# Optimization experiments

Hardware: AMD Instinct MI355X
Metric: run time of the kernel (lower is better)

## Reference

```python
import jax, jax.numpy as jnp
import numpy as np

# Keras Normalization adaption stats for n_neighbors=15 (2*15 = 30 channels)
NORM_MEAN = jnp.array([-3.7189561e-06, 0.000286194, 0.0020740835, 6.5275993, -0.0052857199,
                       10.554636, 0.057773598, 13.915789, 0.060970016, 16.840271,
                       0.0570364, 19.415283, 0.044104282, 21.721455, 0.11490919,
                       23.64683, 0.099816084, 25.365578, 0.01769533, 26.861437,
                       0.054662503, 28.197876, -0.0024771576, 29.295244, 0.039666731,
                       30.319246, 0.0088442909, 31.160933, -0.026727753, 31.874565], dtype=jnp.float32)
NORM_VAR = jnp.array([3.3091978e-06, 0.00016750646, 0.80988622, 85135.219, 1.5621265,
                      222580.2, 8.812871, 386912.78, 10.180468, 566622.44,
                      9.8600769, 753158.06, 7.8372045, 942701.62, 30.926426,
                      1117233.0, 25.045353, 1285543.9, 6.3646226, 1441639.1,
                      12.326629, 1588653.4, 6.9686499, 1714707.9, 10.755516,
                      1836677.8, 8.416419, 1940088.8, 10.344138, 2029969.6], dtype=jnp.float32)
BN_EPS = 1e-3  # keras BatchNormalization default epsilon


def _isc_dirac(x, bc_idx, bc_w, kernel, bias):
    """ConvDirac: barycentric gather-interpolate + rotated template correlation.
    x: (B,V,C); bc_idx/bc_w: (B,V,R,A,3); kernel: (R,A,T,C); bias: (T,)
    returns (B,V,O,T) with O = n_angular rotations (rotation_delta=1)."""
    contrib = jax.vmap(lambda s, i: s[i])(x, bc_idx)            # (B,V,R,A,3,C) gather within batch
    interp = jnp.einsum('bvrat,bvratc->bvrac', bc_w, contrib)    # barycentric interpolation
    n_ang = kernel.shape[1]
    rk = jnp.stack([jnp.roll(kernel, o, axis=1) for o in range(n_ang)])  # (O,R,A,T,C)
    return jax.nn.elu(jnp.einsum('oratc,bvrac->bvot', rk, interp) + bias)


def _amp(x):
    """AngularMaxPooling: pick rotation with maximal euclidean response. x: (B,V,O,T) -> (B,V,T)"""
    idx = jnp.argmax(jnp.linalg.norm(x, axis=-1), axis=-1)       # (B,V)
    return jnp.take_along_axis(x, idx[:, :, None, None], axis=2)[:, :, 0, :]


def _bn(x, gamma, beta):
    # inference-mode BatchNormalization with fresh moving stats (mean=0, var=1)
    return gamma * x * jax.lax.rsqrt(jnp.float32(1.0) + BN_EPS) + beta


def setup_inputs() -> dict:
    key = jax.random.key(0)
    B, V, R, A, K3, C_in = 4, 2048, 5, 8, 3, 30
    dims = [128, 128, 256]
    ks = jax.random.split(key, 16)
    # raw tangent-projection signal, drawn at the scale the adaption stats expect
    signal = NORM_MEAN + jax.random.normal(ks[0], (B, V, C_in), dtype=jnp.float32) * jnp.sqrt(NORM_VAR)
    bc_idx = jax.random.randint(ks[1], (B, V, R, A, K3), 0, V)
    bc_w = jax.random.uniform(ks[2], (B, V, R, A, K3), dtype=jnp.float32)
    bc_w = bc_w / bc_w.sum(axis=-1, keepdims=True)               # barycentric weights sum to 1

    def glorot(k, shape):
        fan = float(np.prod(shape[:-2]) * (shape[-1] + shape[-2])) if len(shape) == 4 else float(shape[0] + shape[1])
        return jax.random.normal(k, shape, dtype=jnp.float32) * jnp.sqrt(2.0 / fan)

    inp = {'signal': signal, 'bc_idx': bc_idx, 'bc_w': bc_w}
    c_prev = C_in
    for i, d in enumerate(dims):
        inp[f'k{i}'] = glorot(ks[3 + i], (R, A, d, c_prev))
        inp[f'b{i}'] = jnp.zeros((d,), jnp.float32)
        inp[f'g{i}'] = jnp.ones((d,), jnp.float32)
        inp[f'be{i}'] = jnp.zeros((d,), jnp.float32)
        c_prev = d
    inp['w1'] = glorot(ks[8], (256, 512)); inp['c1'] = jnp.zeros((512,), jnp.float32)
    inp['w2'] = glorot(ks[9], (512, 256)); inp['c2'] = jnp.zeros((256,), jnp.float32)
    inp['w3'] = glorot(ks[10], (256, 40)); inp['c3'] = jnp.zeros((40,), jnp.float32)
    return inp


def reference(signal, bc_idx, bc_w, k0, b0, g0, be0, k1, b1, g1, be1, k2, b2, g2, be2,
              w1, c1, w2, c2, w3, c3):
    x = (signal - NORM_MEAN) * jax.lax.rsqrt(NORM_VAR)           # input normalization
    for k, b, g, be in ((k0, b0, g0, be0), (k1, b1, g1, be1), (k2, b2, g2, be2)):
        x = _bn(_amp(_isc_dirac(x, bc_idx, bc_w, k, b)), g, be)  # dropout is identity in inference
    x = jnp.max(x, axis=1)                                       # GlobalMaxPool1D over vertices
    x = jax.nn.elu(x @ w1 + c1)
    x = jax.nn.elu(x @ w2 + c2)
    return x @ w3 + c3                                           # (B, 40) logits
```

## Files before the change

kernel.cpp:

```cpp
#include <hip/hip_runtime.h>
#include <hip/hip_bf16.h>
#include <math.h>

#define Bz 4
#define Vz 2048
#define RA 40

typedef short bf16x8 __attribute__((ext_vector_type(8)));
typedef float f32x4 __attribute__((ext_vector_type(4)));

__device__ __forceinline__ unsigned fasu(float f){ union{float f;unsigned u;}x;x.f=f;return x.u; }
__device__ __forceinline__ float usaf(unsigned u){ union{unsigned u;float f;}x;x.u=u;return x.f; }

__device__ __forceinline__ unsigned short f2bf(float f) {
    unsigned u = fasu(f);
    unsigned r = u + 0x7FFF + ((u >> 16) & 1);
    return (unsigned short)(r >> 16);
}
__device__ __forceinline__ float bf2f(unsigned short h) { return usaf(((unsigned)h) << 16); }

__constant__ float NORM_MEAN_C[30] = {
    -3.7189561e-06f, 0.000286194f, 0.0020740835f, 6.5275993f, -0.0052857199f,
    10.554636f, 0.057773598f, 13.915789f, 0.060970016f, 16.840271f,
    0.0570364f, 19.415283f, 0.044104282f, 21.721455f, 0.11490919f,
    23.64683f, 0.099816084f, 25.365578f, 0.01769533f, 26.861437f,
    0.054662503f, 28.197876f, -0.0024771576f, 29.295244f, 0.039666731f,
    30.319246f, 0.0088442909f, 31.160933f, -0.026727753f, 31.874565f};
__constant__ float NORM_VAR_C[30] = {
    3.3091978e-06f, 0.00016750646f, 0.80988622f, 85135.219f, 1.5621265f,
    222580.2f, 8.812871f, 386912.78f, 10.180468f, 566622.44f,
    9.8600769f, 753158.06f, 7.8372045f, 942701.62f, 30.926426f,
    1117233.0f, 25.045353f, 1285543.9f, 6.3646226f, 1441639.1f,
    12.326629f, 1588653.4f, 6.9686499f, 1714707.9f, 10.755516f,
    1836677.8f, 8.416419f, 1940088.8f, 10.344138f, 2029969.6f};

__device__ __forceinline__ float elu_f(float x) {
    return x > 0.f ? x : expm1f(x);
}

__device__ __forceinline__ unsigned encf(float f) {
    unsigned u = fasu(f);
    return (f < 0.f) ? ~u : (u | 0x80000000u);
}
__device__ __forceinline__ float decf(unsigned u) {
    return (u & 0x80000000u) ? usaf(u & 0x7FFFFFFFu) : usaf(~u);
}

template <int CROW, int T, int KB>
__device__ __forceinline__ void expand_body(int e, const float* __restrict__ kern,
                                            unsigned short* __restrict__ wt) {
    constexpr int CB = (CROW == 128) ? 4 : 1;
    int kb = e / (T * 32);
    int rem = e % (T * 32);
    int n = rem >> 5, kk = rem & 31;
    int par = kb & 1;
    int jp = (kb >> 1) & 3;
    int g = kb >> 3;
    int cblk = g % CB;
    int r = g / CB;
    int c = cblk * 32 + kk;
    float v = 0.f;
    if (c < CROW) {
        float k1 = kern[((size_t)((r * 8 + jp) * T + n)) * CROW + c];
        float k2 = kern[((size_t)((r * 8 + jp + 4) * T + n)) * CROW + c];
        v = 0.5f * (par == 0 ? (k1 + k2) : (k1 - k2));
    }
    unsigned short hi = f2bf(v);
    unsigned short lo = f2bf(v - bf2f(hi));
    size_t off = ((size_t)kb * 2) * T * 32 + (n >> 4) * 512 + (kk >> 3) * 128 + (n & 15) * 8 + (kk & 7);
    wt[off] = hi;
    wt[off + (size_t)T * 32] = lo;
}

__global__ void prep_k(const float* __restrict__ sig, float* __restrict__ x0,
                       const float* __restrict__ k0, unsigned short* __restrict__ wt0,
                       const float* __restrict__ k1, unsigned short* __restrict__ wt1,
                       const float* __restrict__ k2, unsigned short* __restrict__ wt2,
                       unsigned* __restrict__ gpool) {
    const int bid = blockIdx.x, tid = threadIdx.x;
    if (bid < 960) {
        int e = bid * 256 + tid;
        if (e < Bz * Vz * 30) {
            int c = e % 30;
            x0[e] = (sig[e] - NORM_MEAN_C[c]) * rsqrtf(NORM_VAR_C[c]);
        }
    } else if (bid < 1600) {
        int e = (bid - 960) * 256 + tid;
        if (e < 40 * 128 * 32) expand_body<30, 128, 40>(e, k0, wt0);
    } else if (bid < 4160) {
        int e = (bid - 1600) * 256 + tid;
        if (e < 160 * 128 * 32) expand_body<128, 128, 160>(e, k1, wt1);
    } else if (bid < 9280) {
        int e = (bid - 4160) * 256 + tid;
        if (e < 160 * 256 * 32) expand_body<128, 256, 160>(e, k2, wt2);
    } else {
        int e = (bid - 9280) * 256 + tid;
        if (e < Bz * 256) gpool[e] = 0u;
    }
}

template <int CROW, int T, int KB, int NW, bool FUSE, bool POOL>
__global__ __launch_bounds__(64 * NW) void conv_k(const float* __restrict__ x,
                                              const int* __restrict__ bc_idx,
                                              const float* __restrict__ bc_w,
                                              const unsigned short* __restrict__ wt,
                                              const float* __restrict__ bias,
                                              const float* __restrict__ g,
                                              const float* __restrict__ be,
                                              float* __restrict__ xout) {
    constexpr int CB = (CROW == 128) ? 4 : 1;
    constexpr int G = KB / 8;
    constexpr int CW = 2 * NW;
    constexpr int CPT = 32 / CW;
    __shared__ unsigned short Ih[2][4096], Il[2][4096];
    __shared__ float normp[64][NW];
    __shared__ int bo[8];
    __shared__ unsigned poolmax[64 * NW];
    const int tid = threadIdx.x;
    const int wid = tid >> 6, lane = tid & 63;
    const int fr = lane & 15, fq = lane >> 4;
    const int fr2 = fr >> 2, om_l = fr & 3;
    const int wn = wid * 64;
    const int m0 = blockIdx.y * 64;
    const int b = m0 >> 14;
    const float* xb_ = x + (size_t)b * Vz * CROW;
    const int* idxb = bc_idx + (size_t)b * Vz * RA * 3;
    const float* wb = bc_w + (size_t)b * Vz * RA * 3;

    const int cidx = tid % CW;
    const int jI = (tid / CW) & 3;
    const int vbI = tid / (CW * 4);
    const int vglob_b = ((m0 & 16383) >> 3) + vbI;
    const int wbase = vbI * 512 + ((cidx * CPT) >> 3) * 128 + ((cidx * CPT) & 7);
    const int nbase = wn >> 4;

    f32x4 acc[4][4] = {};

    auto store_split2 = [&](const float* vv, int buf, int sA, int sB, unsigned sgB) {
        unsigned hp[CPT / 2], lp[CPT / 2];
#pragma unroll
        for (int p2 = 0; p2 < CPT / 2; ++p2) {
            float v0 = vv[2 * p2], v1 = vv[2 * p2 + 1];
            unsigned u0 = fasu(v0), u1 = fasu(v1);
            unsigned h0 = u0 & 0xFFFF0000u, h1 = u1 & 0xFFFF0000u;
            float l0 = v0 - usaf(h0), l1 = v1 - usaf(h1);
            hp[p2] = (u0 >> 16) | h1;
            lp[p2] = (fasu(l0) >> 16) | (fasu(l1) & 0xFFFF0000u);
        }
        auto put = [&](int slot, unsigned sg) {
            const int sl = (slot & 8) | (((slot & 7) + 2 * (vbI & 3)) & 7);
            const int ad = wbase + sl * 8;
            if constexpr (CPT == 8) {
                *(uint4*)&Ih[buf][ad] = make_uint4(hp[0] ^ sg, hp[1] ^ sg, hp[2] ^ sg, hp[3] ^ sg);
                *(uint4*)&Il[buf][ad] = make_uint4(lp[0] ^ sg, lp[1] ^ sg, lp[2] ^ sg, lp[3] ^ sg);
            } else {
                *(uint2*)&Ih[buf][ad] = make_uint2(hp[0] ^ sg, hp[1] ^ sg);
                *(uint2*)&Il[buf][ad] = make_uint2(lp[0] ^ sg, lp[1] ^ sg);
            }
        };
        put(sA, 0u);
        put(sB, sgB);
    };

    int i_n0 = 0, i_n1 = 0, i_n2 = 0, i_n3 = 0, i_n4 = 0, i_n5 = 0;
    float w_n0 = 0.f, w_n1 = 0.f, w_n2 = 0.f, w_n3 = 0.f, w_n4 = 0.f, w_n5 = 0.f;
    {
        const int gi1 = (vglob_b * RA + jI) * 3;
        const int gi2 = gi1 + 12;
        int a0 = idxb[gi1], a1 = idxb[gi1 + 1], a2 = idxb[gi1 + 2];
        int a3 = idxb[gi2], a4 = idxb[gi2 + 1], a5 = idxb[gi2 + 2];
        float u0 = wb[gi1], u1 = wb[gi1 + 1], u2 = wb[gi1 + 2];
        float u3 = wb[gi2], u4 = wb[gi2 + 1], u5 = wb[gi2 + 2];
        float xj[CPT], xj4[CPT];
        const int cs0 = cidx * CPT;
        if (CROW == 128) {
            const float4* p0 = (const float4*)(xb_ + (size_t)a0 * CROW + cs0);
            const float4* p1 = (const float4*)(xb_ + (size_t)a1 * CROW + cs0);
            const float4* p2 = (const float4*)(xb_ + (size_t)a2 * CROW + cs0);
            const float4* p3 = (const float4*)(xb_ + (size_t)a3 * CROW + cs0);
            const float4* p4 = (const float4*)(xb_ + (size_t)a4 * CROW + cs0);
            const float4* p5 = (const float4*)(xb_ + (size_t)a5 * CROW + cs0);
#pragma unroll
            for (int qq = 0; qq < CPT / 4; ++qq) {
                float4 A = p0[qq], B = p1[qq], C = p2[qq];
                xj[qq * 4 + 0] = u0 * A.x + u1 * B.x + u2 * C.x;
                xj[qq * 4 + 1] = u0 * A.y + u1 * B.y + u2 * C.y;
                xj[qq * 4 + 2] = u0 * A.z + u1 * B.z + u2 * C.z;
                xj[qq * 4 + 3] = u0 * A.w + u1 * B.w + u2 * C.w;
                float4 D = p3[qq], E = p4[qq], F = p5[qq];
                xj4[qq * 4 + 0] = u3 * D.x + u4 * E.x + u5 * F.x;
                xj4[qq * 4 + 1] = u3 * D.y + u4 * E.y + u5 * F.y;
                xj4[qq * 4 + 2] = u3 * D.z + u4 * E.z + u5 * F.z;
                xj4[qq * 4 + 3] = u3 * D.w + u4 * E.w + u5 * F.w;
            }
        } else {
#pragma unroll
            for (int cc = 0; cc < CPT; ++cc) {
                int c = cs0 + cc;
                bool ok = (c < CROW);
                xj[cc] = ok ? (u0 * xb_[(size_t)a0 * CROW + c] + u1 * xb_[(size_t)a1 * CROW + c] + u2 * xb_[(size_t)a2 * CROW + c]) : 0.f;
                xj4[cc] = ok ? (u3 * xb_[(size_t)a3 * CROW + c] + u4 * xb_[(size_t)a4 * CROW + c] + u5 * xb_[(size_t)a5 * CROW + c]) : 0.f;
            }
        }
#pragma unroll
        for (int cc = 0; cc < CPT; ++cc) {
            float a_ = xj[cc], b_ = xj4[cc];
            xj[cc] = a_ + b_;
            xj4[cc] = a_ - b_;
        }
        store_split2(xj, 0, jI, jI + 4, 0u);
        store_split2(xj4, 0, 8 + jI, 12 + jI, 0x80008000u);
        if (G > 1) {
            const int rn = 1 / CB;
            const int gi1n = (vglob_b * RA + rn * 8 + jI) * 3;
            const int gi2n = gi1n + 12;
            i_n0 = idxb[gi1n]; i_n1 = idxb[gi1n + 1]; i_n2 = idxb[gi1n + 2];
            i_n3 = idxb[gi2n]; i_n4 = idxb[gi2n + 1]; i_n5 = idxb[gi2n + 2];
            w_n0 = wb[gi1n]; w_n1 = wb[gi1n + 1]; w_n2 = wb[gi1n + 2];
            w_n3 = wb[gi2n]; w_n4 = wb[gi2n + 1]; w_n5 = wb[gi2n + 2];
        }
    }
    __syncthreads();

    for (int gidx = 0; gidx < G; ++gidx) {
        const bool hn = (gidx + 1 < G);
        const int ni0 = i_n0, ni1 = i_n1, ni2 = i_n2, ni3 = i_n3, ni4 = i_n4, ni5 = i_n5;
        const float mw0 = w_n0, mw1 = w_n1, mw2 = w_n2, mw3 = w_n3, mw4 = w_n4, mw5 = w_n5;
        const int bgn = gidx + 1;
        const int cs_n = (bgn % CB) * 32 + cidx * CPT;
        const int ibuf = gidx & 1;
        float4 qa0[CPT / 4], qa1[CPT / 4], qa2[CPT / 4];
        float4 qb0[CPT / 4], qb1[CPT / 4], qb2[CPT / 4];
        float sg[6][CPT];
        float xj[CPT], xj4[CPT];
#pragma unroll
        for (int ap = 0; ap < 8; ++ap) {
            const int jp = ap >> 1, par = ap & 1;
            const int kb = gidx * 8 + ap;
            const unsigned short* bb = wt + ((size_t)kb * 2) * (T * 32) +
                                       (size_t)nbase * 512 + lane * 8;
            bf16x8 bh[4], bl[4];
#pragma unroll
            for (int nj = 0; nj < 4; ++nj) {
                bh[nj] = *(const bf16x8*)(bb + nj * 512);
                bl[nj] = *(const bf16x8*)(bb + (size_t)T * 32 + nj * 512);
            }
            const int sp = (jp + om_l + 2 * fr2) & 7;
            const int sl = par * 8 + sp;
            bf16x8 ah[2], al[2];
#pragma unroll
            for (int miq = 0; miq < 2; ++miq) {
                const int ad = (miq * 4 + fr2) * 512 + fq * 128 + sl * 8;
                ah[miq] = *(const bf16x8*)&Ih[ibuf][ad];
                al[miq] = *(const bf16x8*)&Il[ibuf][ad];
            }
            __builtin_amdgcn_s_setprio(1);
#pragma unroll
            for (int miq = 0; miq < 2; ++miq)
#pragma unroll
                for (int nj = 0; nj < 4; ++nj) {
                    const int mi = par * 2 + miq;
                    acc[mi][nj] = __builtin_amdgcn_mfma_f32_16x16x32_bf16(ah[miq], bh[nj], acc[mi][nj], 0, 0, 0);
                    acc[mi][nj] = __builtin_amdgcn_mfma_f32_16x16x32_bf16(ah[miq], bl[nj], acc[mi][nj], 0, 0, 0);
                    acc[mi][nj] = __builtin_amdgcn_mfma_f32_16x16x32_bf16(al[miq], bh[nj], acc[mi][nj], 0, 0, 0);
                }
            __builtin_amdgcn_s_setprio(0);
            if (hn) {
                if (ap == 0) {
                    if (CROW == 128) {
                        const float4* p0 = (const float4*)(xb_ + (size_t)ni0 * CROW + cs_n);
                        const float4* p1 = (const float4*)(xb_ + (size_t)ni1 * CROW + cs_n);
                        const float4* p2 = (const float4*)(xb_ + (size_t)ni2 * CROW + cs_n);
#pragma unroll
                        for (int qq = 0; qq < CPT / 4; ++qq) { qa0[qq] = p0[qq]; qa1[qq] = p1[qq]; qa2[qq] = p2[qq]; }
                    } else {
#pragma unroll
                        for (int cc = 0; cc < CPT; ++cc) {
                            int c = cs_n + cc;
                            bool ok = (c < CROW);
                            sg[0][cc] = ok ? xb_[(size_t)ni0 * CROW + c] : 0.f;
                            sg[1][cc] = ok ? xb_[(size_t)ni1 * CROW + c] : 0.f;
                            sg[2][cc] = ok ? xb_[(size_t)ni2 * CROW + c] : 0.f;
                        }
                    }
                } else if (ap == 1) {
                    if (CROW == 128) {
                        const float4* p3 = (const float4*)(xb_ + (size_t)ni3 * CROW + cs_n);
                        const float4* p4 = (const float4*)(xb_ + (size_t)ni4 * CROW + cs_n);
                        const float4* p5 = (const float4*)(xb_ + (size_t)ni5 * CROW + cs_n);
#pragma unroll
                        for (int qq = 0; qq < CPT / 4; ++qq) { qb0[qq] = p3[qq]; qb1[qq] = p4[qq]; qb2[qq] = p5[qq]; }
                    } else {
#pragma unroll
                        for (int cc = 0; cc < CPT; ++cc) {
                            int c = cs_n + cc;
                            bool ok = (c < CROW);
                            sg[3][cc] = ok ? xb_[(size_t)ni3 * CROW + c] : 0.f;
                            sg[4][cc] = ok ? xb_[(size_t)ni4 * CROW + c] : 0.f;
                            sg[5][cc] = ok ? xb_[(size_t)ni5 * CROW + c] : 0.f;
                        }
                    }
                } else if (ap == 2) {
                    if (gidx + 2 < G) {
                        const int rn = (gidx + 2) / CB;
                        const int gi1 = (vglob_b * RA + rn * 8 + jI) * 3;
                        const int gi2 = gi1 + 12;
                        i_n0 = idxb[gi1]; i_n1 = idxb[gi1 + 1]; i_n2 = idxb[gi1 + 2];
                        i_n3 = idxb[gi2]; i_n4 = idxb[gi2 + 1]; i_n5 = idxb[gi2 + 2];
                        w_n0 = wb[gi1]; w_n1 = wb[gi1 + 1]; w_n2 = wb[gi1 + 2];
                        w_n3 = wb[gi2]; w_n4 = wb[gi2 + 1]; w_n5 = wb[gi2 + 2];
                    }
                } else if (ap == 3) {
                    if (CROW == 128) {
#pragma unroll
                        for (int qq = 0; qq < CPT / 4; ++qq) {
                            float4 A = qa0[qq], B = qa1[qq], C = qa2[qq];
                            xj[qq * 4 + 0] = mw0 * A.x + mw1 * B.x + mw2 * C.x;
                            xj[qq * 4 + 1] = mw0 * A.y + mw1 * B.y + mw2 * C.y;
                            xj[qq * 4 + 2] = mw0 * A.z + mw1 * B.z + mw2 * C.z;
                            xj[qq * 4 + 3] = mw0 * A.w + mw1 * B.w + mw2 * C.w;
                        }
                    } else {
#pragma unroll
                        for (int cc = 0; cc < CPT; ++cc)
                            xj[cc] = mw0 * sg[0][cc] + mw1 * sg[1][cc] + mw2 * sg[2][cc];
                    }
                } else if (ap == 4) {
                    if (CROW == 128) {
#pragma unroll
                        for (int qq = 0; qq < CPT / 4; ++qq) {
                            float4 D = qb0[qq], E = qb1[qq], F = qb2[qq];
                            xj4[qq * 4 + 0] = mw3 * D.x + mw4 * E.x + mw5 * F.x;
                            xj4[qq * 4 + 1] = mw3 * D.y + mw4 * E.y + mw5 * F.y;
                            xj4[qq * 4 + 2] = mw3 * D.z + mw4 * E.z + mw5 * F.z;
                            xj4[qq * 4 + 3] = mw3 * D.w + mw4 * E.w + mw5 * F.w;
                        }
                    } else {
#pragma unroll
                        for (int cc = 0; cc < CPT; ++cc)
                            xj4[cc] = mw3 * sg[3][cc] + mw4 * sg[4][cc] + mw5 * sg[5][cc];
                    }
                } else if (ap == 5) {
#pragma unroll
                    for (int cc = 0; cc < CPT; ++cc) {
                        float a_ = xj[cc], b_ = xj4[cc];
                        xj[cc] = a_ + b_;
                        xj4[cc] = a_ - b_;
                    }
                } else if (ap == 6) {
                    store_split2(xj, ibuf ^ 1, jI, jI + 4, 0u);
                } else {
                    store_split2(xj4, ibuf ^ 1, 8 + jI, 12 + jI, 0x80008000u);
                }
            }
        }
        __syncthreads();
    }

    if (FUSE) {
        float ssP[2][4], ssM[2][4];
#pragma unroll
        for (int mg = 0; mg < 2; ++mg)
#pragma unroll
            for (int r = 0; r < 4; ++r) { ssP[mg][r] = 0.f; ssM[mg][r] = 0.f; }
#pragma unroll
        for (int mg = 0; mg < 2; ++mg)
#pragma unroll
            for (int nj = 0; nj < 4; ++nj)
#pragma unroll
                for (int r = 0; r < 4; ++r) {
                    const int t = wn + nj * 16 + fr;
                    float se = acc[mg][nj][r], so = acc[mg + 2][nj][r];
                    float vP = elu_f(se + so + bias[t]);
                    float vM = elu_f(se - so + bias[t]);
                    acc[mg][nj][r] = vP;
                    acc[mg + 2][nj][r] = vM;
                    ssP[mg][r] += vP * vP;
                    ssM[mg][r] += vM * vM;
                }
#pragma unroll
        for (int mg = 0; mg < 2; ++mg)
#pragma unroll
            for (int r = 0; r < 4; ++r) {
                float s1 = ssP[mg][r];
                s1 += __shfl_xor(s1, 1); s1 += __shfl_xor(s1, 2);
                s1 += __shfl_xor(s1, 4); s1 += __shfl_xor(s1, 8);
                float s2 = ssM[mg][r];
                s2 += __shfl_xor(s2, 1); s2 += __shfl_xor(s2, 2);
                s2 += __shfl_xor(s2, 4); s2 += __shfl_xor(s2, 8);
                if (fr == 0) {
                    normp[(mg * 4 + fq) * 8 + r][wid] = s1;
                    normp[(mg * 4 + fq) * 8 + r + 4][wid] = s2;
                }
            }
        __syncthreads();
        if (POOL) poolmax[tid] = 0u;
        if (tid < 8) {
            float best = -1.f; int bsel = 0;
#pragma unroll
            for (int oo = 0; oo < 8; ++oo) {
                float tot = 0.f;
#pragma unroll
                for (int wq = 0; wq < NW; ++wq) tot += normp[tid * 8 + oo][wq];
                if (tot > best) { best = tot; bsel = oo; }
            }
            bo[tid] = bsel;
        }
        __syncthreads();
        const float rsbn = rsqrtf(1.001f);
#pragma unroll
        for (int mg = 0; mg < 2; ++mg)
#pragma unroll
            for (int r = 0; r < 4; ++r) {
                const int vloc = mg * 4 + fq;
                const int bsel = bo[vloc];
                if (r == bsel) {
                    const int vg = (m0 >> 3) + vloc;
#pragma unroll
                    for (int nj = 0; nj < 4; ++nj) {
                        const int t = wn + nj * 16 + fr;
                        float f = acc[mg][nj][r] * g[t] * rsbn + be[t];
                        if (!POOL) xout[(size_t)vg * T + t] = f;
                        else atomicMax(&poolmax[t], encf(f));
                    }
                }
                if (r + 4 == bsel) {
                    const int vg = (m0 >> 3) + vloc;
#pragma unroll
                    for (int nj = 0; nj < 4; ++nj) {
                        const int t = wn + nj * 16 + fr;
                        float f = acc[mg + 2][nj][r] * g[t] * rsbn + be[t];
                        if (!POOL) xout[(size_t)vg * T + t] = f;
                        else atomicMax(&poolmax[t], encf(f));
                    }
                }
            }
        if (POOL) {
            __syncthreads();
            unsigned pv = poolmax[tid];
            if (pv) atomicMax((unsigned*)xout + (((size_t)b) << 8) + tid, pv);
        }
    }
}

__global__ __launch_bounds__(256) void head_k(const float* __restrict__ partial,
                                              const float* __restrict__ w1, const float* __restrict__ c1,
                                              const float* __restrict__ w2, const float* __restrict__ c2,
                                              const float* __restrict__ w3, const float* __restrict__ c3,
                                              float* __restrict__ outp) {
    __shared__ float p[256], h1s[512], h2s[256];
    const int b = blockIdx.x, tid = threadIdx.x;
    const unsigned* gp = (const unsigned*)partial;
    p[tid] = decf(gp[b * 256 + tid]);
    __syncthreads();
#pragma unroll
    for (int rep = 0; rep < 2; ++rep) {
        int n = rep * 256 + tid;
        float s = c1[n];
        for (int k = 0; k < 256; ++k) s += p[k] * w1[k * 512 + n];
        h1s[n] = elu_f(s);
    }
    __syncthreads();
    {
        float s = c2[tid];
        for (int k = 0; k < 512; ++k) s += h1s[k] * w2[k * 256 + tid];
        h2s[tid] = elu_f(s);
    }
    __syncthreads();
    if (tid < 40) {
        float s = c3[tid];
        for (int k = 0; k < 256; ++k) s += h2s[k] * w3[k * 40 + tid];
        outp[b * 40 + tid] = s;
    }
}

extern "C" void kernel_launch(void* const* d_in, const int* in_sizes, int n_in,
                              void* d_out, int out_size, void* d_ws, size_t ws_size,
                              hipStream_t stream) {
    const float* signal = (const float*)d_in[0];
    const int* bc_idx = (const int*)d_in[1];
    const float* bc_w = (const float*)d_in[2];
    const float* k0 = (const float*)d_in[3];
    const float* b0 = (const float*)d_in[4];
    const float* g0 = (const float*)d_in[5];
    const float* be0 = (const float*)d_in[6];
    const float* k1 = (const float*)d_in[7];
    const float* b1 = (const float*)d_in[8];
    const float* g1 = (const float*)d_in[9];
    const float* be1 = (const float*)d_in[10];
    const float* k2 = (const float*)d_in[11];
    const float* b2 = (const float*)d_in[12];
    const float* g2 = (const float*)d_in[13];
    const float* be2 = (const float*)d_in[14];
    const float* w1 = (const float*)d_in[15];
    const float* c1 = (const float*)d_in[16];
    const float* w2 = (const float*)d_in[17];
    const float* c2 = (const float*)d_in[18];
    const float* w3 = (const float*)d_in[19];
    const float* c3 = (const float*)d_in[20];
    float* outp = (float*)d_out;

    float* ws = (float*)d_ws;
    float* xa = ws;
    float* xb = xa + (size_t)8192 * 128;
    unsigned* gpool = (unsigned*)(xb + (size_t)8192 * 128);
    unsigned short* wt0 = (unsigned short*)(gpool + 4096);
    unsigned short* wt1 = wt0 + (size_t)40 * 2 * 128 * 32;
    unsigned short* wt2 = wt1 + (size_t)160 * 2 * 128 * 32;

    prep_k<<<9284, 256, 0, stream>>>(signal, xa, k0, wt0, k1, wt1, k2, wt2, gpool);

    conv_k<30, 128, 40, 2, true, false><<<dim3(1, 1024), 128, 0, stream>>>(
        xa, bc_idx, bc_w, wt0, b0, g0, be0, xb);

    conv_k<128, 128, 160, 2, true, false><<<dim3(1, 1024), 128, 0, stream>>>(
        xb, bc_idx, bc_w, wt1, b1, g1, be1, xa);

    conv_k<128, 256, 160, 4, true, true><<<dim3(1, 1024), 256, 0, stream>>>(
        xa, bc_idx, bc_w, wt2, b2, g2, be2, (float*)gpool);

    head_k<<<Bz, 256, 0, stream>>>((const float*)gpool, w1, c1, w2, c2, w3, c3, outp);
}
```

Before: 577.7 us.

## Process two M-tiles per block in layer-3 conv to reuse weight fragments

```diff
diff --git a/kernel.cpp b/kernel.cpp
--- a/kernel.cpp
+++ b/kernel.cpp
@@ -99,8 +99,8 @@
     }
 }
 
-template <int CROW, int T, int KB, int NW, bool FUSE, bool POOL>
-__global__ __launch_bounds__(64 * NW) void conv_k(const float* __restrict__ x,
+template <int CROW, int T, int KB, int NW, int MT, bool FUSE, bool POOL>
+__global__ __launch_bounds__(64 * NW, 2) void conv_k(const float* __restrict__ x,
                                               const int* __restrict__ bc_idx,
                                               const float* __restrict__ bc_w,
                                               const unsigned short* __restrict__ wt,
@@ -110,18 +110,18 @@
                                               float* __restrict__ xout) {
     constexpr int CB = (CROW == 128) ? 4 : 1;
     constexpr int G = KB / 8;
-    constexpr int CW = 2 * NW;
+    constexpr int CW = 2 * NW / MT;
     constexpr int CPT = 32 / CW;
-    __shared__ unsigned short Ih[2][4096], Il[2][4096];
-    __shared__ float normp[64][NW];
-    __shared__ int bo[8];
+    __shared__ unsigned short Ih[2][4096 * MT], Il[2][4096 * MT];
+    __shared__ float normp[64 * MT][NW];
+    __shared__ int bo[8 * MT];
     __shared__ unsigned poolmax[64 * NW];
     const int tid = threadIdx.x;
     const int wid = tid >> 6, lane = tid & 63;
     const int fr = lane & 15, fq = lane >> 4;
     const int fr2 = fr >> 2, om_l = fr & 3;
     const int wn = wid * 64;
-    const int m0 = blockIdx.y * 64;
+    const int m0 = blockIdx.y * (64 * MT);
     const int b = m0 >> 14;
     const float* xb_ = x + (size_t)b * Vz * CROW;
     const int* idxb = bc_idx + (size_t)b * Vz * RA * 3;
@@ -134,7 +134,7 @@
     const int wbase = vbI * 512 + ((cidx * CPT) >> 3) * 128 + ((cidx * CPT) & 7);
     const int nbase = wn >> 4;
 
-    f32x4 acc[4][4] = {};
+    f32x4 acc[MT][4][4] = {};
 
     auto store_split2 = [&](const float* vv, int buf, int sA, int sB, unsigned sgB) {
         unsigned hp[CPT / 2], lp[CPT / 2];
@@ -247,24 +247,27 @@
             }
             const int sp = (jp + om_l + 2 * fr2) & 7;
             const int sl = par * 8 + sp;
-            bf16x8 ah[2], al[2];
-#pragma unroll
-            for (int miq = 0; miq < 2; ++miq) {
-                const int ad = (miq * 4 + fr2) * 512 + fq * 128 + sl * 8;
-                ah[miq] = *(const bf16x8*)&Ih[ibuf][ad];
-                al[miq] = *(const bf16x8*)&Il[ibuf][ad];
-            }
-            __builtin_amdgcn_s_setprio(1);
-#pragma unroll
-            for (int miq = 0; miq < 2; ++miq)
-#pragma unroll
-                for (int nj = 0; nj < 4; ++nj) {
-                    const int mi = par * 2 + miq;
-                    acc[mi][nj] = __builtin_amdgcn_mfma_f32_16x16x32_bf16(ah[miq], bh[nj], acc[mi][nj], 0, 0, 0);
-                    acc[mi][nj] = __builtin_amdgcn_mfma_f32_16x16x32_bf16(ah[miq], bl[nj], acc[mi][nj], 0, 0, 0);
-                    acc[mi][nj] = __builtin_amdgcn_mfma_f32_16x16x32_bf16(al[miq], bh[nj], acc[mi][nj], 0, 0, 0);
+#pragma unroll
+            for (int mt = 0; mt < MT; ++mt) {
+                bf16x8 ah[2], al[2];
+#pragma unroll
+                for (int miq = 0; miq < 2; ++miq) {
+                    const int ad = mt * 4096 + (miq * 4 + fr2) * 512 + fq * 128 + sl * 8;
+                    ah[miq] = *(const bf16x8*)&Ih[ibuf][ad];
+                    al[miq] = *(const bf16x8*)&Il[ibuf][ad];
                 }
-            __builtin_amdgcn_s_setprio(0);
+                __builtin_amdgcn_s_setprio(1);
+#pragma unroll
+                for (int miq = 0; miq < 2; ++miq)
+#pragma unroll
+                    for (int nj = 0; nj < 4; ++nj) {
+                        const int mi = par * 2 + miq;
+                        acc[mt][mi][nj] = __builtin_amdgcn_mfma_f32_16x16x32_bf16(ah[miq], bh[nj], acc[mt][mi][nj], 0, 0, 0);
+                        acc[mt][mi][nj] = __builtin_amdgcn_mfma_f32_16x16x32_bf16(ah[miq], bl[nj], acc[mt][mi][nj], 0, 0, 0);
+                        acc[mt][mi][nj] = __builtin_amdgcn_mfma_f32_16x16x32_bf16(al[miq], bh[nj], acc[mt][mi][nj], 0, 0, 0);
+                    }
+                __builtin_amdgcn_s_setprio(0);
+            }
             if (hn) {
                 if (ap == 0) {
                     if (CROW == 128) {
@@ -358,44 +361,50 @@
     }
 
     if (FUSE) {
-        float ssP[2][4], ssM[2][4];
-#pragma unroll
-        for (int mg = 0; mg < 2; ++mg)
-#pragma unroll
-            for (int r = 0; r < 4; ++r) { ssP[mg][r] = 0.f; ssM[mg][r] = 0.f; }
-#pragma unroll
-        for (int mg = 0; mg < 2; ++mg)
-#pragma unroll
-            for (int nj = 0; nj < 4; ++nj)
+        float ssP[MT][2][4], ssM[MT][2][4];
+#pragma unroll
+        for (int mt = 0; mt < MT; ++mt)
+#pragma unroll
+            for (int mg = 0; mg < 2; ++mg)
+#pragma unroll
+                for (int r = 0; r < 4; ++r) { ssP[mt][mg][r] = 0.f; ssM[mt][mg][r] = 0.f; }
+#pragma unroll
+        for (int mt = 0; mt < MT; ++mt)
+#pragma unroll
+            for (int mg = 0; mg < 2; ++mg)
+#pragma unroll
+                for (int nj = 0; nj < 4; ++nj)
+#pragma unroll
+                    for (int r = 0; r < 4; ++r) {
+                        const int t = wn + nj * 16 + fr;
+                        float se = acc[mt][mg][nj][r], so = acc[mt][mg + 2][nj][r];
+                        float vP = elu_f(se + so + bias[t]);
+                        float vM = elu_f(se - so + bias[t]);
+                        acc[mt][mg][nj][r] = vP;
+                        acc[mt][mg + 2][nj][r] = vM;
+                        ssP[mt][mg][r] += vP * vP;
+                        ssM[mt][mg][r] += vM * vM;
+                    }
+#pragma unroll
+        for (int mt = 0; mt < MT; ++mt)
+#pragma unroll
+            for (int mg = 0; mg < 2; ++mg)
 #pragma unroll
                 for (int r = 0; r < 4; ++r) {
-                    const int t = wn + nj * 16 + fr;
-                    float se = acc[mg][nj][r], so = acc[mg + 2][nj][r];
-                    float vP = elu_f(se + so + bias[t]);
-                    float vM = elu_f(se - so + bias[t]);
-                    acc[mg][nj][r] = vP;
-                    acc[mg + 2][nj][r] = vM;
-                    ssP[mg][r] += vP * vP;
-                    ssM[mg][r] += vM * vM;
+                    float s1 = ssP[mt][mg][r];
+                    s1 += __shfl_xor(s1, 1); s1 += __shfl_xor(s1, 2);
+                    s1 += __shfl_xor(s1, 4); s1 += __shfl_xor(s1, 8);
+                    float s2 = ssM[mt][mg][r];
+                    s2 += __shfl_xor(s2, 1); s2 += __shfl_xor(s2, 2);
+                    s2 += __shfl_xor(s2, 4); s2 += __shfl_xor(s2, 8);
+                    if (fr == 0) {
+                        normp[(mt * 8 + mg * 4 + fq) * 8 + r][wid] = s1;
+                        normp[(mt * 8 + mg * 4 + fq) * 8 + r + 4][wid] = s2;
+                    }
                 }
-#pragma unroll
-        for (int mg = 0; mg < 2; ++mg)
-#pragma unroll
-            for (int r = 0; r < 4; ++r) {
-                float s1 = ssP[mg][r];
-                s1 += __shfl_xor(s1, 1); s1 += __shfl_xor(s1, 2);
-                s1 += __shfl_xor(s1, 4); s1 += __shfl_xor(s1, 8);
-                float s2 = ssM[mg][r];
-                s2 += __shfl_xor(s2, 1); s2 += __shfl_xor(s2, 2);
-                s2 += __shfl_xor(s2, 4); s2 += __shfl_xor(s2, 8);
-                if (fr == 0) {
-                    normp[(mg * 4 + fq) * 8 + r][wid] = s1;
-                    normp[(mg * 4 + fq) * 8 + r + 4][wid] = s2;
-                }
-            }
         __syncthreads();
         if (POOL) poolmax[tid] = 0u;
-        if (tid < 8) {
+        if (tid < 8 * MT) {
             float best = -1.f; int bsel = 0;
 #pragma unroll
             for (int oo = 0; oo < 8; ++oo) {
@@ -409,32 +418,34 @@
         __syncthreads();
         const float rsbn = rsqrtf(1.001f);
 #pragma unroll
-        for (int mg = 0; mg < 2; ++mg)
-#pragma unroll
-            for (int r = 0; r < 4; ++r) {
-                const int vloc = mg * 4 + fq;
-                const int bsel = bo[vloc];
-                if (r == bsel) {
-                    const int vg = (m0 >> 3) + vloc;
-#pragma unroll
-                    for (int nj = 0; nj < 4; ++nj) {
-                        const int t = wn + nj * 16 + fr;
-                        float f = acc[mg][nj][r] * g[t] * rsbn + be[t];
-                        if (!POOL) xout[(size_t)vg * T + t] = f;
-                        else atomicMax(&poolmax[t], encf(f));
+        for (int mt = 0; mt < MT; ++mt)
+#pragma unroll
+            for (int mg = 0; mg < 2; ++mg)
+#pragma unroll
+                for (int r = 0; r < 4; ++r) {
+                    const int vloc = mt * 8 + mg * 4 + fq;
+                    const int bsel = bo[vloc];
+                    if (r == bsel) {
+                        const int vg = (m0 >> 3) + vloc;
+#pragma unroll
+                        for (int nj = 0; nj < 4; ++nj) {
+                            const int t = wn + nj * 16 + fr;
+                            float f = acc[mt][mg][nj][r] * g[t] * rsbn + be[t];
+                            if (!POOL) xout[(size_t)vg * T + t] = f;
+                            else atomicMax(&poolmax[t], encf(f));
+                        }
+                    }
+                    if (r + 4 == bsel) {
+                        const int vg = (m0 >> 3) + vloc;
+#pragma unroll
+                        for (int nj = 0; nj < 4; ++nj) {
+                            const int t = wn + nj * 16 + fr;
+                            float f = acc[mt][mg + 2][nj][r] * g[t] * rsbn + be[t];
+                            if (!POOL) xout[(size_t)vg * T + t] = f;
+                            else atomicMax(&poolmax[t], encf(f));
+                        }
                     }
                 }
-                if (r + 4 == bsel) {
-                    const int vg = (m0 >> 3) + vloc;
-#pragma unroll
-                    for (int nj = 0; nj < 4; ++nj) {
-                        const int t = wn + nj * 16 + fr;
-                        float f = acc[mg + 2][nj][r] * g[t] * rsbn + be[t];
-                        if (!POOL) xout[(size_t)vg * T + t] = f;
-                        else atomicMax(&poolmax[t], encf(f));
-                    }
-                }
-            }
         if (POOL) {
             __syncthreads();
             unsigned pv = poolmax[tid];
@@ -510,13 +521,13 @@
 
     prep_k<<<9284, 256, 0, stream>>>(signal, xa, k0, wt0, k1, wt1, k2, wt2, gpool);
 
-    conv_k<30, 128, 40, 2, true, false><<<dim3(1, 1024), 128, 0, stream>>>(
+    conv_k<30, 128, 40, 2, 1, true, false><<<dim3(1, 1024), 128, 0, stream>>>(
         xa, bc_idx, bc_w, wt0, b0, g0, be0, xb);
 
-    conv_k<128, 128, 160, 2, true, false><<<dim3(1, 1024), 128, 0, stream>>>(
+    conv_k<128, 128, 160, 2, 1, true, false><<<dim3(1, 1024), 128, 0, stream>>>(
         xb, bc_idx, bc_w, wt1, b1, g1, be1, xa);
 
-    conv_k<128, 256, 160, 4, true, true><<<dim3(1, 1024), 256, 0, stream>>>(
+    conv_k<128, 256, 160, 4, 2, true, true><<<dim3(1, 512), 256, 0, stream>>>(
         xa, bc_idx, bc_w, wt2, b2, g2, be2, (float*)gpool);
 
     head_k<<<Bz, 256, 0, stream>>>((const float*)gpool, w1, c1, w2, c2, w3, c3, outp);
```

Result: slower. 616.0 us (+6.6%).
